# Kernel optimization log

Hardware: AMD Instinct MI355X
Metric: run time of the kernel (lower is better)

## Reference

```python
import jax, jax.numpy as jnp
import numpy as np

LN_EPS = 1e-5
LOCAL_SIZE = 256
N_HEAD, D_HEAD = 16, 64


def layer_norm_c(x):
    # layer norm over channel dim (axis=1), no affine params (matches F.layer_norm(x.T,(d,)).T)
    m = jnp.mean(x, axis=1, keepdims=True)
    v = jnp.var(x, axis=1, keepdims=True)
    return (x - m) / jnp.sqrt(v + LN_EPS)


def rel_shift(x):
    # x: [b, n, q, k] -> Transformer-XL relative shift
    b, n, q, k = x.shape
    x = jnp.pad(x, ((0, 0), (0, 0), (0, 0), (1, 0)))
    return x.reshape(b, n, k + 1, q)[:, :, 1:].reshape(b, n, q, k)


def setup_inputs() -> dict:
    key = jax.random.key(0)
    ks = jax.random.split(key, 14)
    bsz, d_model, qlen, mlen = 4, 1024, 512, 512
    klen = qlen + mlen
    d_inner = 4096
    s = lambda k, shape, sc=0.05: jax.random.normal(k, shape, dtype=jnp.float32) * sc
    return {
        "z1ss": jax.random.normal(ks[0], (bsz, d_model, qlen), dtype=jnp.float32),
        "uss": jax.random.normal(ks[1], (bsz, 3 * d_model, klen), dtype=jnp.float32) * 0.1,
        "z0": jax.random.normal(ks[2], (bsz, d_model, mlen), dtype=jnp.float32),
        "pos_emb": jax.random.normal(ks[3], (1, d_model, klen), dtype=jnp.float32),
        "qkv_w": s(ks[4], (3 * d_model, d_model)),
        "r_w": s(ks[5], (d_model, d_model)),
        "r_w_bias": s(ks[6], (N_HEAD, D_HEAD)),
        "r_r_bias": s(ks[7], (N_HEAD, D_HEAD)),
        "o_w": s(ks[8], (d_model, d_model)),
        "o_b": s(ks[9], (d_model,)),
        "ff1_w": s(ks[10], (d_inner, d_model)),
        "ff1_b": s(ks[11], (d_inner,)),
        "ff2_w": s(ks[12], (d_model, d_inner)),
        "ff2_b": s(ks[13], (d_model,)),
    }


def reference(z1ss, uss, z0, pos_emb, qkv_w, r_w, r_w_bias, r_r_bias, o_w, o_b,
              ff1_w, ff1_b, ff2_w, ff2_b):
    bsz, d_model, qlen = z1ss.shape
    mlen = z0.shape[2]
    n_head, d_head = N_HEAD, D_HEAD
    scale = 1.0 / d_head ** 0.5

    # ---- self-attention (post-lnorm path) ----
    cat = jnp.concatenate([z0, z1ss], axis=-1)              # [b, d, klen]
    klen = cat.shape[2]
    w_heads = jnp.einsum('od,bdk->bok', qkv_w, cat) + uss   # [b, 3d, klen]
    r_head_k = jnp.einsum('od,dk->ok', r_w, pos_emb[0])     # [d, rlen]
    rlen = r_head_k.shape[1]

    w_head_q, w_head_k, w_head_v = jnp.split(w_heads, 3, axis=1)
    w_head_q = w_head_q[:, :, -qlen:]
    w_head_q = w_head_q.reshape(bsz, n_head, d_head, qlen)
    w_head_k = w_head_k.reshape(bsz, n_head, d_head, klen)
    w_head_v = w_head_v.reshape(bsz, n_head, d_head, klen)
    r_head_k = r_head_k.reshape(n_head, d_head, rlen)

    rw_q = w_head_q + r_w_bias[:, :, None]                  # [b,n,d,q]
    AC = jnp.einsum('bndi,bndj->bnij', rw_q, w_head_k)      # [b,n,q,k]
    rr_q = w_head_q + r_r_bias[:, :, None]
    BD = rel_shift(jnp.einsum('bndi,ndj->bnij', rr_q, r_head_k))
    attn_score = (AC + BD) * scale

    local_size = LOCAL_SIZE if LOCAL_SIZE else 1000
    i = jnp.arange(qlen)[:, None]
    j = jnp.arange(klen)[None, :]
    mask = (j > i + mlen) | (j <= i + mlen - local_size)    # causal + local window
    attn_score = jnp.where(mask[None, None], -jnp.inf, attn_score)

    attn_prob = jax.nn.softmax(attn_score, axis=-1)
    attn_vec = jnp.einsum('bnij,bndj->bndi', attn_prob, w_head_v)
    attn_vec = attn_vec.reshape(bsz, n_head * d_head, qlen)
    attn_out = jnp.einsum('od,bdq->boq', o_w, attn_vec) + o_b[None, :, None]
    x = layer_norm_c(attn_out + z1ss)                       # post-lnorm

    # ---- position-wise FF (weight-shared, post-lnorm) ----
    h = jax.nn.relu(jnp.einsum('id,bdq->biq', ff1_w, x) + ff1_b[None, :, None])
    out2 = jnp.einsum('di,biq->bdq', ff2_w, h) + ff2_b[None, :, None]
    return layer_norm_c(out2 + x)
```

## Files before the change

### kernel.cpp

```cpp
#include <hip/hip_runtime.h>
#include <hip/hip_bf16.h>

typedef unsigned short u16;
typedef __attribute__((ext_vector_type(8))) short s8v;
typedef __attribute__((ext_vector_type(4))) short s4v;
typedef __attribute__((ext_vector_type(4))) float f4v;

__device__ __forceinline__ float s2f(u16 s) {
    unsigned int u = ((unsigned int)s) << 16;
    return __builtin_bit_cast(float, u);
}
__device__ __forceinline__ u16 f2s(float f) {
    __hip_bfloat16 h = __float2bfloat16(f);
    return __builtin_bit_cast(u16, h);
}

__device__ __forceinline__ void gl2lds16(const u16* g, u16* l) {
    __builtin_amdgcn_global_load_lds((const __attribute__((address_space(1))) void*)g,
                                     (__attribute__((address_space(3))) void*)l, 16, 0, 0);
}

#define BSZ 4
#define DM 1024
#define QLEN 512
#define MLEN 512
#define KLEN 1024
#define DI 4096
#define NH 16
#define DH 64
#define WIN 256

__global__ __launch_bounds__(256) void conv_w5(
    const float* __restrict__ s0, const float* __restrict__ s1,
    const float* __restrict__ s2, const float* __restrict__ s3,
    const float* __restrict__ s4,
    u16* __restrict__ d0, u16* __restrict__ d1, u16* __restrict__ d2,
    u16* __restrict__ d3, u16* __restrict__ d4)
{
    const int e0 = 786432, e1 = e0 + 262144, e2 = e1 + 262144,
              e3 = e2 + 1048576, e4 = e3 + 1048576;
    int i = blockIdx.x * 256 + threadIdx.x;
    const float* s; u16* d; int off;
    if (i < e0)      { s = s0; d = d0; off = i; }
    else if (i < e1) { s = s1; d = d1; off = i - e0; }
    else if (i < e2) { s = s2; d = d2; off = i - e1; }
    else if (i < e3) { s = s3; d = d3; off = i - e2; }
    else if (i < e4) { s = s4; d = d4; off = i - e3; }
    else return;
    f4v v = *(const f4v*)&s[(size_t)off * 4];
    s4v o;
#pragma unroll
    for (int k = 0; k < 4; ++k) o[k] = (short)f2s(v[k]);
    *(s4v*)&d[(size_t)off * 4] = o;
}

__global__ __launch_bounds__(256) void trans_f2b(
    const float* __restrict__ src, long sS, int ldS, int colOff,
    u16* __restrict__ dst, long sD, int ldD, int rowOff)
{
    __shared__ float tile[32][33];
    int b = blockIdx.z;
    int t0 = blockIdx.x * 32, f0 = blockIdx.y * 32;
    int tx = threadIdx.x, ty = threadIdx.y;
#pragma unroll
    for (int p = 0; p < 4; ++p)
        tile[ty + 8 * p][tx] = src[(size_t)b * sS + (size_t)(f0 + ty + 8 * p) * ldS + colOff + t0 + tx];
    __syncthreads();
#pragma unroll
    for (int p = 0; p < 4; ++p)
        dst[(size_t)b * sD + (size_t)(rowOff + t0 + ty + 8 * p) * ldD + f0 + tx] = f2s(tile[tx][ty + 8 * p]);
}

__global__ __launch_bounds__(256) void uss_add(
    const float* __restrict__ uss, u16* __restrict__ whT, u16* __restrict__ vT)
{
    __shared__ float tile[32][33];
    int b = blockIdx.z;
    int t0 = blockIdx.x * 32, fy = blockIdx.y;
    int tx = threadIdx.x, ty = threadIdx.y;
    const float* S = uss + (size_t)b * 3072 * 1024;
    if (fy < 64) {
        int f0 = fy * 32;
        u16* D = whT + (size_t)b * 1024 * 3072;
#pragma unroll
        for (int p = 0; p < 4; ++p)
            tile[ty + 8 * p][tx] = S[(size_t)(f0 + ty + 8 * p) * 1024 + t0 + tx];
        __syncthreads();
#pragma unroll
        for (int p = 0; p < 4; ++p) {
            size_t o = (size_t)(t0 + ty + 8 * p) * 3072 + f0 + tx;
            D[o] = f2s(s2f(D[o]) + tile[tx][ty + 8 * p]);
        }
    } else {
        int d0 = (fy - 64) * 32;
#pragma unroll
        for (int p = 0; p < 4; ++p) {
            int d = d0 + ty + 8 * p;
            size_t ui = ((size_t)2048 + d) * 1024 + t0 + tx;
            size_t vi = (size_t)d * 4096 + (size_t)b * KLEN + t0 + tx;
            vT[vi] = f2s(s2f(vT[vi]) + S[ui]);
        }
    }
}

__global__ __launch_bounds__(256) void trans_b2f(
    const u16* __restrict__ src, long sS, int ldS,
    float* __restrict__ dst, long sD, int ldD)
{
    __shared__ float tile[32][33];
    int b = blockIdx.z;
    int t0 = blockIdx.x * 32, f0 = blockIdx.y * 32;
    int tx = threadIdx.x, ty = threadIdx.y;
#pragma unroll
    for (int p = 0; p < 4; ++p)
        tile[ty + 8 * p][tx] = s2f(src[(size_t)b * sS + (size_t)(f0 + ty + 8 * p) * ldS + t0 + tx]);
    __syncthreads();
#pragma unroll
    for (int p = 0; p < 4; ++p)
        dst[(size_t)b * sD + (size_t)(t0 + ty + 8 * p) * ldD + f0 + tx] = tile[tx][ty + 8 * p];
}

template<int BN, int SPLIT>
__global__ __launch_bounds__(256) void gemm_bt(
    const u16* __restrict__ A,
    const u16* __restrict__ B,
    u16* __restrict__ C,
    float* __restrict__ fOut,
    int M, int K,
    const float* __restrict__ bias,
    int relu,
    long pstride,
    u16* __restrict__ vTout)
{
    constexpr int BM = 128, BK = 64;
    constexpr int MI = (BN == 128) ? 4 : 2;
    constexpr int NI = 4;
    const int n0 = blockIdx.x * BN, m0 = blockIdx.y * BM;
    const int Ks = K / SPLIT;
    const int kbeg = blockIdx.z * Ks;
    __shared__ __align__(16) u16 As[BM * BK];
    __shared__ __align__(16) u16 Bs[BN * BK];
    const int tid = threadIdx.x, lane = tid & 63, wv = tid >> 6;
    const int l15 = lane & 15, quad = lane >> 4;
    const int wm = (BN == 128) ? (wv >> 1) * 64 : wv * 32;
    const int wn = (BN == 128) ? (wv & 1) * 64 : 0;
    f4v acc[MI][NI] = {};
    for (int kk = kbeg; kk < kbeg + Ks; kk += BK) {
        __syncthreads();
#pragma unroll
        for (int p = 0; p < (BM * 8) / 256; ++p) {
            int c = p * 256 + tid, r = c >> 3, q = c & 7, qs = q ^ (r & 7);
            gl2lds16(&A[(size_t)(m0 + r) * K + kk + qs * 8], &As[c * 8]);
        }
#pragma unroll
        for (int p = 0; p < (BN * 8) / 256; ++p) {
            int c = p * 256 + tid, r = c >> 3, q = c & 7, qs = q ^ (r & 7);
            gl2lds16(&B[(size_t)(n0 + r) * K + kk + qs * 8], &Bs[c * 8]);
        }
        __syncthreads();
#pragma unroll
        for (int k0 = 0; k0 < BK; k0 += 32) {
            s8v af[MI], bf[NI];
#pragma unroll
            for (int mi = 0; mi < MI; ++mi) {
                int r = wm + mi * 16 + l15;
                af[mi] = *(const s8v*)&As[r * BK + ((((k0 >> 3) + quad) ^ (r & 7)) << 3)];
            }
#pragma unroll
            for (int ni = 0; ni < NI; ++ni) {
                int r = wn + ni * 16 + l15;
                bf[ni] = *(const s8v*)&Bs[r * BK + ((((k0 >> 3) + quad) ^ (r & 7)) << 3)];
            }
#pragma unroll
            for (int mi = 0; mi < MI; ++mi)
#pragma unroll
                for (int ni = 0; ni < NI; ++ni)
                    acc[mi][ni] = __builtin_amdgcn_mfma_f32_16x16x32_bf16(af[mi], bf[ni], acc[mi][ni], 0, 0, 0);
        }
    }
    if (SPLIT > 1) {
        float* base = fOut + (long)blockIdx.z * pstride;
#pragma unroll
        for (int mi = 0; mi < MI; ++mi) {
            int m = m0 + wm + mi * 16 + quad * 4;
#pragma unroll
            for (int ni = 0; ni < NI; ++ni) {
                int n = n0 + wn + ni * 16 + l15;
                *(f4v*)&base[(size_t)n * M + m] = acc[mi][ni];
            }
        }
    } else if (vTout && m0 >= 2048) {
#pragma unroll
        for (int mi = 0; mi < MI; ++mi) {
            int m = m0 + wm + mi * 16 + quad * 4;
#pragma unroll
            for (int ni = 0; ni < NI; ++ni) {
                int n = n0 + wn + ni * 16 + l15;
#pragma unroll
                for (int r2 = 0; r2 < 4; ++r2)
                    vTout[(size_t)(m + r2 - 2048) * 4096 + n] = f2s(acc[mi][ni][r2]);
            }
        }
    } else {
#pragma unroll
        for (int mi = 0; mi < MI; ++mi) {
            int m = m0 + wm + mi * 16 + quad * 4;
            float bv[4] = {0.f, 0.f, 0.f, 0.f};
            if (bias) {
#pragma unroll
                for (int r2 = 0; r2 < 4; ++r2) bv[r2] = bias[m + r2];
            }
#pragma unroll
            for (int ni = 0; ni < NI; ++ni) {
                int n = n0 + wn + ni * 16 + l15;
                float o[4];
#pragma unroll
                for (int r2 = 0; r2 < 4; ++r2) o[r2] = acc[mi][ni][r2] + bv[r2];
                if (relu) {
#pragma unroll
                    for (int r2 = 0; r2 < 4; ++r2) o[r2] = fmaxf(o[r2], 0.f);
                }
                s4v st;
#pragma unroll
                for (int r2 = 0; r2 < 4; ++r2) st[r2] = (short)f2s(o[r2]);
                *(s4v*)&C[(size_t)n * M + m] = st;
            }
        }
    }
}

#define QT 16
#define SROW 260
__global__ __launch_bounds__(256, 4) void attn_mfma(
    const u16* __restrict__ WHT,
    const u16* __restrict__ VT,
    const u16* __restrict__ RT,
    const float* __restrict__ rwb, const float* __restrict__ rrb,
    u16* __restrict__ avT)
{
    __shared__ __align__(16) float sS[QT * SROW];

    const int qt = blockIdx.x, n = blockIdx.y, b = blockIdx.z;
    const int i0 = qt * QT, j0 = i0 + WIN + 1;
    const int tid = threadIdx.x, lane = tid & 63, wv = tid >> 6;
    const int l15 = lane & 15, quad = lane >> 4;
    const u16* W = WHT + (size_t)b * KLEN * (3 * DM);

    s8v qac[2], qbd[2];
    {
        int qrow = MLEN + i0 + l15;
#pragma unroll
        for (int kc = 0; kc < 2; ++kc) {
            int col = n * DH + kc * 32 + quad * 8;
            s8v qv = *(const s8v*)&W[(size_t)qrow * (3 * DM) + col];
            s8v a, c;
#pragma unroll
            for (int e = 0; e < 8; ++e) {
                float qf = s2f((u16)qv[e]);
                a[e] = (short)f2s(qf + rwb[col + e]);
                c[e] = (short)f2s(qf + rrb[col + e]);
            }
            qac[kc] = a; qbd[kc] = c;
        }
    }

    for (int ci = wv; ci < 17; ci += 4) {
        f4v acc = {};
        const u16* Kr = &W[(size_t)(j0 + ci * 16 + l15) * (3 * DM) + DM + n * DH + quad * 8];
        acc = __builtin_amdgcn_mfma_f32_16x16x32_bf16(qac[0], *(const s8v*)Kr, acc, 0, 0, 0);
        acc = __builtin_amdgcn_mfma_f32_16x16x32_bf16(qac[1], *(const s8v*)(Kr + 32), acc, 0, 0, 0);
#pragma unroll
        for (int r2 = 0; r2 < 4; ++r2) {
            int qi = quad * 4 + r2;
            int t = ci * 16 + l15 - qi;
            if ((unsigned)t < 256u) sS[qi * SROW + t] = acc[r2];
        }
    }
    __syncthreads();

#pragma unroll
    for (int cc = 0; cc < 4; ++cc) {
        int ci = wv + cc * 4;
        f4v acc = {};
        const u16* Rr = &RT[(size_t)(ci * 16 + l15) * DM + n * DH + quad * 8];
        acc = __builtin_amdgcn_mfma_f32_16x16x32_bf16(qbd[0], *(const s8v*)Rr, acc, 0, 0, 0);
        acc = __builtin_amdgcn_mfma_f32_16x16x32_bf16(qbd[1], *(const s8v*)(Rr + 32), acc, 0, 0, 0);
#pragma unroll
        for (int r2 = 0; r2 < 4; ++r2) {
            int qi = quad * 4 + r2;
            sS[qi * SROW + ci * 16 + l15] += acc[r2];
        }
    }
    __syncthreads();

    {
        int g = tid >> 4, l = tid & 15;
        float vals[16], mx = -1e30f;
#pragma unroll
        for (int k = 0; k < 16; ++k) {
            float s = sS[g * SROW + l + 16 * k] * 0.125f;
            vals[k] = s; mx = fmaxf(mx, s);
        }
        asm volatile("" ::: "memory");
#pragma unroll
        for (int d = 1; d < 16; d <<= 1) mx = fmaxf(mx, __shfl_xor(mx, d, 16));
        float sum = 0.f;
#pragma unroll
        for (int k = 0; k < 16; ++k) { vals[k] = __expf(vals[k] - mx); sum += vals[k]; }
#pragma unroll
        for (int d = 1; d < 16; d <<= 1) sum += __shfl_xor(sum, d, 16);
        float inv = 1.f / sum;
        u16* sPr = (u16*)&sS[g * SROW];
#pragma unroll
        for (int k = 0; k < 16; ++k) sPr[g + 1 + l + 16 * k] = f2s(vals[k] * inv);
        sPr[l <= g ? l : 256 + l] = 0;
        sPr[272 + l] = 0;
    }
    __syncthreads();

    const u16* sPu = (const u16*)sS;
    const size_t vbase = (size_t)(n * DH + wv * 16 + l15) * 4096
                       + (size_t)b * KLEN + (j0 - 1) + quad * 8;
    f4v o = {};
#pragma unroll
    for (int kc = 0; kc < 9; ++kc) {
        size_t vi = vbase + kc * 32;
        if (vi > (size_t)4194304 - 8) vi = (size_t)4194304 - 8;
        s8v a  = *(const s8v*)&sPu[(size_t)l15 * (2 * SROW) + kc * 32 + quad * 8];
        s8v bb = *(const s8v*)&VT[vi];
        o = __builtin_amdgcn_mfma_f32_16x16x32_bf16(a, bb, o, 0, 0, 0);
    }
#pragma unroll
    for (int r2 = 0; r2 < 4; ++r2) {
        int qi = quad * 4 + r2;
        avT[((size_t)b * QLEN + i0 + qi) * DM + n * DH + wv * 16 + l15] = f2s(o[r2]);
    }
}

__global__ __launch_bounds__(256) void ln_f(
    const float* __restrict__ P, long pstride, int nparts,
    const float* __restrict__ bias,
    const u16* __restrict__ res, int resMode, u16* __restrict__ out)
{
    int n = blockIdx.x, tid = threadIdx.x;
    int lane = tid & 63, wv = tid >> 6;
    int f = tid * 4;
    int rrow = resMode ? (((n >> 9) * 2 + 1) * 512 + (n & 511)) : n;
    f4v pv = *(const f4v*)&P[(size_t)n * DM + f];
    for (int p = 1; p < nparts; ++p) {
        const float* Pp = P + (long)p * pstride;
        pv += *(const f4v*)&Pp[(size_t)n * DM + f];
    }
    s4v rv = *(const s4v*)&res[(size_t)rrow * DM + f];
    f4v bv = *(const f4v*)&bias[f];
    float v[4];
#pragma unroll
    for (int k = 0; k < 4; ++k) v[k] = pv[k] + bv[k] + s2f((u16)rv[k]);
    float s = v[0] + v[1] + v[2] + v[3];
    float ss = v[0] * v[0] + v[1] * v[1] + v[2] * v[2] + v[3] * v[3];
#pragma unroll
    for (int d = 1; d < 64; d <<= 1) {
        s += __shfl_xor(s, d, 64);
        ss += __shfl_xor(ss, d, 64);
    }
    __shared__ float ps[4], pss[4];
    if (lane == 0) { ps[wv] = s; pss[wv] = ss; }
    __syncthreads();
    float S = ps[0] + ps[1] + ps[2] + ps[3];
    float SS = pss[0] + pss[1] + pss[2] + pss[3];
    float m = S * (1.f / DM);
    float var = SS * (1.f / DM) - m * m;
    float inv = rsqrtf(fmaxf(var, 0.f) + 1e-5f);
    s4v st;
#pragma unroll
    for (int k = 0; k < 4; ++k) st[k] = (short)f2s((v[k] - m) * inv);
    *(s4v*)&out[(size_t)n * DM + f] = st;
}

extern "C" void kernel_launch(void* const* d_in, const int* in_sizes, int n_in,
                              void* d_out, int out_size, void* d_ws, size_t ws_size,
                              hipStream_t stream) {
    const float* z1ss  = (const float*)d_in[0];
    const float* uss   = (const float*)d_in[1];
    const float* z0    = (const float*)d_in[2];
    const float* pos   = (const float*)d_in[3];
    const float* qkv_w = (const float*)d_in[4];
    const float* r_w   = (const float*)d_in[5];
    const float* rwb   = (const float*)d_in[6];
    const float* rrb   = (const float*)d_in[7];
    const float* o_w   = (const float*)d_in[8];
    const float* o_b   = (const float*)d_in[9];
    const float* ff1_w = (const float*)d_in[10];
    const float* ff1_b = (const float*)d_in[11];
    const float* ff2_w = (const float*)d_in[12];
    const float* ff2_b = (const float*)d_in[13];

    u16* ws = (u16*)d_ws;
    u16* wQ   = ws;
    u16* wR   = ws + 3145728;
    u16* wO   = ws + 4194304;
    u16* wF1  = ws + 5242880;
    u16* wF2  = ws + 9437184;
    u16* catT = ws + 13631488;
    u16* whT  = ws + 17825792;
    u16* posT = ws + 30408704;
    u16* rT   = ws + 30670848;
    u16* avT  = ws + 30932992;
    u16* xT   = ws + 33030144;
    float* pref = (float*)(ws + 35127296);
    u16* hT   = whT;
    u16* outT = catT;

    u16* vT = (u16*)pref;

    float* part1 = (float*)d_ws;
    long pstr = part1 - pref;

    dim3 tblk(32, 8);

    conv_w5<<<13312, 256, 0, stream>>>(qkv_w, r_w, o_w, ff1_w, ff2_w,
                                       wQ, wR, wO, wF1, wF2);

    trans_f2b<<<dim3(16, 32, BSZ), tblk, 0, stream>>>(z0, (long)DM * MLEN, MLEN, 0,
                                                      catT, (long)KLEN * DM, DM, 0);
    trans_f2b<<<dim3(16, 32, BSZ), tblk, 0, stream>>>(z1ss, (long)DM * QLEN, QLEN, 0,
                                                      catT, (long)KLEN * DM, DM, MLEN);
    trans_f2b<<<dim3(8, 32, 1), tblk, 0, stream>>>(pos, 0, KLEN, KLEN - WIN,
                                                   posT, 0, DM, 0);

    gemm_bt<64, 1><<<dim3(64, 24, 1), 256, 0, stream>>>(
        wQ, catT, whT, nullptr, 3 * DM, DM, nullptr, 0, 0, vT);

    uss_add<<<dim3(32, 96, BSZ), tblk, 0, stream>>>(uss, whT, vT);

    gemm_bt<64, 1><<<dim3(4, 8, 1), 256, 0, stream>>>(
        wR, posT, rT, nullptr, DM, DM, nullptr, 0, 0, nullptr);

    attn_mfma<<<dim3(QLEN / QT, NH, BSZ), 256, 0, stream>>>(whT, vT, rT, rwb, rrb, avT);

    gemm_bt<64, 2><<<dim3(32, 8, 2), 256, 0, stream>>>(
        wO, avT, nullptr, pref, DM, DM, nullptr, 0, pstr, nullptr);

    ln_f<<<2048, 256, 0, stream>>>(pref, pstr, 2, o_b, catT, 1, xT);

    gemm_bt<64, 1><<<dim3(32, 32, 1), 256, 0, stream>>>(
        wF1, xT, hT, nullptr, DI, DM, ff1_b, 1, 0, nullptr);

    gemm_bt<64, 2><<<dim3(32, 8, 2), 256, 0, stream>>>(
        wF2, hT, nullptr, pref, DM, DI, nullptr, 0, pstr, nullptr);

    ln_f<<<2048, 256, 0, stream>>>(pref, pstr, 2, ff2_b, xT, 0, outT);

    trans_b2f<<<dim3(32, 16, BSZ), tblk, 0, stream>>>(outT, (long)QLEN * DM, DM,
                                                      (float*)d_out, (long)DM * QLEN, QLEN);
}
```

Measured before the change: 347.0 us.

## Skip unused QKV query rows for memory tokens and process 32 queries per attention block

The QKV GEMM now returns early for tiles that produce query features (rows below 1024) at memory-token positions (first 512 of each batch), since only the last qlen queries are used. uss_add skips the matching region. The attention kernel doubles its query tile to 32 rows, reusing each loaded K, R and V fragment across two MFMA row groups, and launches half as many blocks. This cuts redundant GEMM work and global loads, at the cost of more registers per thread and fewer blocks in the attention kernel.

```diff
diff --git a/kernel.cpp b/kernel.cpp
--- a/kernel.cpp
+++ b/kernel.cpp
@@ -78,6 +78,7 @@
     int b = blockIdx.z;
     int t0 = blockIdx.x * 32, fy = blockIdx.y;
     int tx = threadIdx.x, ty = threadIdx.y;
+    if (fy < 32 && t0 < 512) return;
     const float* S = uss + (size_t)b * 3072 * 1024;
     if (fy < 64) {
         int f0 = fy * 32;
@@ -129,6 +130,7 @@
     int M, int K,
     const float* __restrict__ bias,
     int relu,
+    int qskip,
     long pstride,
     u16* __restrict__ vTout)
 {
@@ -136,6 +138,7 @@
     constexpr int MI = (BN == 128) ? 4 : 2;
     constexpr int NI = 4;
     const int n0 = blockIdx.x * BN, m0 = blockIdx.y * BM;
+    if (qskip && m0 + BM <= 1024 && (n0 & 1023) < 512) return;
     const int Ks = K / SPLIT;
     const int kbeg = blockIdx.z * Ks;
     __shared__ __align__(16) u16 As[BM * BK];
@@ -229,7 +232,7 @@
     }
 }
 
-#define QT 16
+#define QT 32
 #define SROW 260
 __global__ __launch_bounds__(256, 4) void attn_mfma(
     const u16* __restrict__ WHT,
@@ -246,9 +249,10 @@
     const int l15 = lane & 15, quad = lane >> 4;
     const u16* W = WHT + (size_t)b * KLEN * (3 * DM);
 
-    s8v qac[2], qbd[2];
-    {
-        int qrow = MLEN + i0 + l15;
+    s8v qac[2][2], qbd[2][2];
+#pragma unroll
+    for (int h = 0; h < 2; ++h) {
+        int qrow = MLEN + i0 + 16 * h + l15;
 #pragma unroll
         for (int kc = 0; kc < 2; ++kc) {
             int col = n * DH + kc * 32 + quad * 8;
@@ -260,20 +264,25 @@
                 a[e] = (short)f2s(qf + rwb[col + e]);
                 c[e] = (short)f2s(qf + rrb[col + e]);
             }
-            qac[kc] = a; qbd[kc] = c;
-        }
-    }
-
-    for (int ci = wv; ci < 17; ci += 4) {
-        f4v acc = {};
-        const u16* Kr = &W[(size_t)(j0 + ci * 16 + l15) * (3 * DM) + DM + n * DH + quad * 8];
-        acc = __builtin_amdgcn_mfma_f32_16x16x32_bf16(qac[0], *(const s8v*)Kr, acc, 0, 0, 0);
-        acc = __builtin_amdgcn_mfma_f32_16x16x32_bf16(qac[1], *(const s8v*)(Kr + 32), acc, 0, 0, 0);
-#pragma unroll
-        for (int r2 = 0; r2 < 4; ++r2) {
-            int qi = quad * 4 + r2;
-            int t = ci * 16 + l15 - qi;
-            if ((unsigned)t < 256u) sS[qi * SROW + t] = acc[r2];
+            qac[h][kc] = a; qbd[h][kc] = c;
+        }
+    }
+
+    for (int ci = wv; ci < 18; ci += 4) {
+        int j = j0 + ci * 16 + l15; if (j > KLEN - 1) j = KLEN - 1;
+        const u16* Kr = &W[(size_t)j * (3 * DM) + DM + n * DH + quad * 8];
+        s8v k0 = *(const s8v*)Kr, k1 = *(const s8v*)(Kr + 32);
+#pragma unroll
+        for (int h = 0; h < 2; ++h) {
+            f4v acc = {};
+            acc = __builtin_amdgcn_mfma_f32_16x16x32_bf16(qac[h][0], k0, acc, 0, 0, 0);
+            acc = __builtin_amdgcn_mfma_f32_16x16x32_bf16(qac[h][1], k1, acc, 0, 0, 0);
+#pragma unroll
+            for (int r2 = 0; r2 < 4; ++r2) {
+                int qi = 16 * h + quad * 4 + r2;
+                int t = ci * 16 + l15 - qi;
+                if ((unsigned)t < 256u) sS[qi * SROW + t] = acc[r2];
+            }
         }
     }
     __syncthreads();
@@ -281,59 +290,72 @@
 #pragma unroll
     for (int cc = 0; cc < 4; ++cc) {
         int ci = wv + cc * 4;
-        f4v acc = {};
         const u16* Rr = &RT[(size_t)(ci * 16 + l15) * DM + n * DH + quad * 8];
-        acc = __builtin_amdgcn_mfma_f32_16x16x32_bf16(qbd[0], *(const s8v*)Rr, acc, 0, 0, 0);
-        acc = __builtin_amdgcn_mfma_f32_16x16x32_bf16(qbd[1], *(const s8v*)(Rr + 32), acc, 0, 0, 0);
-#pragma unroll
-        for (int r2 = 0; r2 < 4; ++r2) {
-            int qi = quad * 4 + r2;
-            sS[qi * SROW + ci * 16 + l15] += acc[r2];
+        s8v r0 = *(const s8v*)Rr, r1 = *(const s8v*)(Rr + 32);
+#pragma unroll
+        for (int h = 0; h < 2; ++h) {
+            f4v acc = {};
+            acc = __builtin_amdgcn_mfma_f32_16x16x32_bf16(qbd[h][0], r0, acc, 0, 0, 0);
+            acc = __builtin_amdgcn_mfma_f32_16x16x32_bf16(qbd[h][1], r1, acc, 0, 0, 0);
+#pragma unroll
+            for (int r2 = 0; r2 < 4; ++r2) {
+                int qi = 16 * h + quad * 4 + r2;
+                sS[qi * SROW + ci * 16 + l15] += acc[r2];
+            }
         }
     }
     __syncthreads();
 
     {
         int g = tid >> 4, l = tid & 15;
-        float vals[16], mx = -1e30f;
-#pragma unroll
-        for (int k = 0; k < 16; ++k) {
-            float s = sS[g * SROW + l + 16 * k] * 0.125f;
-            vals[k] = s; mx = fmaxf(mx, s);
-        }
-        asm volatile("" ::: "memory");
-#pragma unroll
-        for (int d = 1; d < 16; d <<= 1) mx = fmaxf(mx, __shfl_xor(mx, d, 16));
-        float sum = 0.f;
-#pragma unroll
-        for (int k = 0; k < 16; ++k) { vals[k] = __expf(vals[k] - mx); sum += vals[k]; }
-#pragma unroll
-        for (int d = 1; d < 16; d <<= 1) sum += __shfl_xor(sum, d, 16);
-        float inv = 1.f / sum;
-        u16* sPr = (u16*)&sS[g * SROW];
-#pragma unroll
-        for (int k = 0; k < 16; ++k) sPr[g + 1 + l + 16 * k] = f2s(vals[k] * inv);
-        sPr[l <= g ? l : 256 + l] = 0;
-        sPr[272 + l] = 0;
+#pragma unroll
+        for (int h = 0; h < 2; ++h) {
+            int r = g + 16 * h;
+            float vals[16], mx = -1e30f;
+#pragma unroll
+            for (int k = 0; k < 16; ++k) {
+                float s = sS[r * SROW + l + 16 * k] * 0.125f;
+                vals[k] = s; mx = fmaxf(mx, s);
+            }
+            asm volatile("" ::: "memory");
+#pragma unroll
+            for (int d = 1; d < 16; d <<= 1) mx = fmaxf(mx, __shfl_xor(mx, d, 16));
+            float sum = 0.f;
+#pragma unroll
+            for (int k = 0; k < 16; ++k) { vals[k] = __expf(vals[k] - mx); sum += vals[k]; }
+#pragma unroll
+            for (int d = 1; d < 16; d <<= 1) sum += __shfl_xor(sum, d, 16);
+            float inv = 1.f / sum;
+            u16* sPr = (u16*)&sS[r * SROW];
+#pragma unroll
+            for (int k = 0; k < 16; ++k) sPr[r + 1 + l + 16 * k] = f2s(vals[k] * inv);
+            if (l <= r) sPr[l] = 0;
+            if (l + 16 <= r) sPr[l + 16] = 0;
+            int p = r + 257 + l;
+            if (p < 288) sPr[p] = 0;
+            p += 16;
+            if (p < 288) sPr[p] = 0;
+        }
     }
     __syncthreads();
 
     const u16* sPu = (const u16*)sS;
     const size_t vbase = (size_t)(n * DH + wv * 16 + l15) * 4096
                        + (size_t)b * KLEN + (j0 - 1) + quad * 8;
-    f4v o = {};
+    f4v o0 = {}, o1 = {};
 #pragma unroll
     for (int kc = 0; kc < 9; ++kc) {
-        size_t vi = vbase + kc * 32;
-        if (vi > (size_t)4194304 - 8) vi = (size_t)4194304 - 8;
-        s8v a  = *(const s8v*)&sPu[(size_t)l15 * (2 * SROW) + kc * 32 + quad * 8];
-        s8v bb = *(const s8v*)&VT[vi];
-        o = __builtin_amdgcn_mfma_f32_16x16x32_bf16(a, bb, o, 0, 0, 0);
+        s8v bb = *(const s8v*)&VT[vbase + kc * 32];
+        s8v a0 = *(const s8v*)&sPu[(size_t)l15 * (2 * SROW) + kc * 32 + quad * 8];
+        s8v a1 = *(const s8v*)&sPu[(size_t)(16 + l15) * (2 * SROW) + kc * 32 + quad * 8];
+        o0 = __builtin_amdgcn_mfma_f32_16x16x32_bf16(a0, bb, o0, 0, 0, 0);
+        o1 = __builtin_amdgcn_mfma_f32_16x16x32_bf16(a1, bb, o1, 0, 0, 0);
     }
 #pragma unroll
     for (int r2 = 0; r2 < 4; ++r2) {
         int qi = quad * 4 + r2;
-        avT[((size_t)b * QLEN + i0 + qi) * DM + n * DH + wv * 16 + l15] = f2s(o[r2]);
+        avT[((size_t)b * QLEN + i0 + qi) * DM + n * DH + wv * 16 + l15] = f2s(o0[r2]);
+        avT[((size_t)b * QLEN + i0 + 16 + qi) * DM + n * DH + wv * 16 + l15] = f2s(o1[r2]);
     }
 }
 
@@ -429,25 +451,25 @@
                                                    posT, 0, DM, 0);
 
     gemm_bt<64, 1><<<dim3(64, 24, 1), 256, 0, stream>>>(
-        wQ, catT, whT, nullptr, 3 * DM, DM, nullptr, 0, 0, vT);
+        wQ, catT, whT, nullptr, 3 * DM, DM, nullptr, 0, 1, 0, vT);
 
     uss_add<<<dim3(32, 96, BSZ), tblk, 0, stream>>>(uss, whT, vT);
 
     gemm_bt<64, 1><<<dim3(4, 8, 1), 256, 0, stream>>>(
-        wR, posT, rT, nullptr, DM, DM, nullptr, 0, 0, nullptr);
+        wR, posT, rT, nullptr, DM, DM, nullptr, 0, 0, 0, nullptr);
 
     attn_mfma<<<dim3(QLEN / QT, NH, BSZ), 256, 0, stream>>>(whT, vT, rT, rwb, rrb, avT);
 
     gemm_bt<64, 2><<<dim3(32, 8, 2), 256, 0, stream>>>(
-        wO, avT, nullptr, pref, DM, DM, nullptr, 0, pstr, nullptr);
+        wO, avT, nullptr, pref, DM, DM, nullptr, 0, 0, pstr, nullptr);
 
     ln_f<<<2048, 256, 0, stream>>>(pref, pstr, 2, o_b, catT, 1, xT);
 
     gemm_bt<64, 1><<<dim3(32, 32, 1), 256, 0, stream>>>(
-        wF1, xT, hT, nullptr, DI, DM, ff1_b, 1, 0, nullptr);
+        wF1, xT, hT, nullptr, DI, DM, ff1_b, 1, 0, 0, nullptr);
 
     gemm_bt<64, 2><<<dim3(32, 8, 2), 256, 0, stream>>>(
-        wF2, hT, nullptr, pref, DM, DI, nullptr, 0, pstr, nullptr);
+        wF2, hT, nullptr, pref, DM, DI, nullptr, 0, 0, pstr, nullptr);
 
     ln_f<<<2048, 256, 0, stream>>>(pref, pstr, 2, ff2_b, xT, 0, outT);
 
```

New measurement: 337.5 us. 1.03x faster.
